# Performance work log

Hardware: AMD Instinct MI355X
Metric: run time of the kernel (lower is better)

The kernel has to match this reference:

```python
import jax, jax.numpy as jnp
import numpy as np

HEAD_NUM = 16
EMBED = 1024
B, T = 2, 2048


def setup_inputs() -> dict:
    key = jax.random.key(0)
    k1, k2, k3 = jax.random.split(key, 3)
    x = jax.random.normal(k1, (B, T, EMBED), dtype=jnp.float32)
    # torch Linear weights: [out_features, in_features]; scaled like default init
    w_qkv = jax.random.normal(k2, (3 * EMBED, EMBED), dtype=jnp.float32) / np.sqrt(EMBED)
    w_out = jax.random.normal(k3, (EMBED, EMBED), dtype=jnp.float32) / np.sqrt(EMBED)
    return {"x": x, "w_qkv": w_qkv, "w_out": w_out}


def reference(x, w_qkv, w_out):
    b, t, e = x.shape
    h = HEAD_NUM
    d = e // h
    dk = d ** 0.5  # NOTE: original MULTIPLIES scores by sqrt(head_dim)
    qkv = x @ w_qkv.T  # [b, t, 3e]
    # einops 'b t (d k h) -> k b h t d' with k=3: split order is (d, 3, h)
    qkv = qkv.reshape(b, t, d, 3, h)
    qkv = jnp.transpose(qkv, (3, 0, 4, 1, 2))  # [3, b, h, t, d]
    q, k, v = qkv[0], qkv[1], qkv[2]
    energy = jnp.einsum('bhid,bhjd->bhij', q, k) * dk  # [b, h, t, t]
    attn = jax.nn.softmax(energy, axis=-1)
    out = jnp.einsum('bhij,bhjd->bhid', attn, v)  # [b, h, t, d]
    out = jnp.transpose(out, (0, 2, 1, 3)).reshape(b, t, e)  # b t (h d)
    return out @ w_out.T
```

## Files before the change

### kernel.cpp

```cpp
#include <hip/hip_runtime.h>
#include <hip/hip_bf16.h>

typedef _Float16 f16x8 __attribute__((ext_vector_type(8)));
typedef unsigned short u16x8 __attribute__((ext_vector_type(8)));
typedef unsigned short u16x4 __attribute__((ext_vector_type(4)));
typedef float f32x4 __attribute__((ext_vector_type(4)));

static constexpr int Bn = 2;
static constexpr int Tn = 2048;
static constexpr int En = 1024;
static constexpr int Hn = 16;
static constexpr int Dn = 64;
#define LOG2E 1.44269504088896340736f

static constexpr int TS = 136;
static constexpr int PS = 40;

__device__ __forceinline__ unsigned short f2h(float x) {
  _Float16 h = (_Float16)x;
  return __builtin_bit_cast(unsigned short, h);
}
__device__ __forceinline__ float h2f(unsigned short u) {
  return (float)__builtin_bit_cast(_Float16, u);
}
__device__ __forceinline__ f16x8 ldh8(const unsigned short* p) {
  return __builtin_bit_cast(f16x8, *reinterpret_cast<const u16x8*>(p));
}
__device__ __forceinline__ unsigned int pk2(float a, float b) {
  return __builtin_bit_cast(unsigned int, __builtin_amdgcn_cvt_pkrtz(a, b));
}
__device__ __forceinline__ void gld16(const void* g, void* l) {
  __builtin_amdgcn_global_load_lds(
      (__attribute__((address_space(1))) void*)(const_cast<void*>(g)),
      (__attribute__((address_space(3))) void*)(l), 16, 0, 0);
}

__global__ __launch_bounds__(256) void split_f32_f16(
    const float* __restrict__ src, unsigned short* __restrict__ hi,
    unsigned short* __restrict__ lo)
{
  const int i = (blockIdx.x * 256 + threadIdx.x) * 4;
  const float4 v = *reinterpret_cast<const float4*>(src + i);
  ushort4 h, l;
  h.x = f2h(v.x); l.x = f2h(v.x - h2f(h.x));
  h.y = f2h(v.y); l.y = f2h(v.y - h2f(h.y));
  h.z = f2h(v.z); l.z = f2h(v.z - h2f(h.z));
  h.w = f2h(v.w); l.w = f2h(v.w - h2f(h.w));
  *reinterpret_cast<ushort4*>(hi + i) = h;
  *reinterpret_cast<ushort4*>(lo + i) = l;
}

__global__ __launch_bounds__(256) void cvt_f32_f16(
    const float* __restrict__ src, unsigned short* __restrict__ dst)
{
  const int i = (blockIdx.x * 256 + threadIdx.x) * 4;
  const float4 v = *reinterpret_cast<const float4*>(src + i);
  ushort4 u;
  u.x = f2h(v.x); u.y = f2h(v.y); u.z = f2h(v.z); u.w = f2h(v.w);
  *reinterpret_cast<ushort4*>(dst + i) = u;
}

__global__ __launch_bounds__(256) void gemm_qkv(
    const unsigned short* __restrict__ xh, const unsigned short* __restrict__ xl,
    const unsigned short* __restrict__ wf,
    unsigned short* __restrict__ Qf, unsigned short* __restrict__ Kf,
    unsigned short* __restrict__ Vf, int M, int K)
{
  __shared__ unsigned short smem[2 * 12288];

  const int tid = threadIdx.x;
  const int w = tid >> 6, L = tid & 63, qd = L >> 4, lr = L & 15;
  const int m0 = blockIdx.y * 128;
  const int kk = blockIdx.x >> 3;
  const int hh0 = (blockIdx.x & 7) * 2;
  const int wm = (w >> 1) * 64, wn = (w & 1) * 64;

  size_t aoffs[2], boffs[2];
  int lbase[2];
#pragma unroll
  for (int p = 0; p < 2; ++p) {
    const int c = p * 256 + tid;
    const int row = c >> 2, slot = c & 3;
    const int dd = row & 63, hl = row >> 6;
    aoffs[p] = (size_t)(m0 + row) * K + slot * 8;
    boffs[p] = (size_t)(dd * 48 + kk * 16 + hh0 + hl) * K + slot * 8;
    lbase[p] = (p * 4 + w) * 512;
  }

  f32x4 acc[4][4] = {};

#pragma unroll
  for (int p = 0; p < 2; ++p) {
    gld16(xh + aoffs[p], &smem[lbase[p]]);
    gld16(wf + boffs[p], &smem[8192 + lbase[p]]);
    if (kk < 2) gld16(xl + aoffs[p], &smem[4096 + lbase[p]]);
  }
  __syncthreads();

  int buf = 0;
  for (int k0 = 0; k0 < K; k0 += 32) {
    if (k0 + 32 < K) {
      const int nb = (buf ^ 1) * 12288;
#pragma unroll
      for (int p = 0; p < 2; ++p) {
        gld16(xh + aoffs[p] + k0 + 32, &smem[nb + lbase[p]]);
        gld16(wf + boffs[p] + k0 + 32, &smem[nb + 8192 + lbase[p]]);
        if (kk < 2) gld16(xl + aoffs[p] + k0 + 32, &smem[nb + 4096 + lbase[p]]);
      }
    }

    const int cb = buf * 12288;
    f16x8 afh[4], bf[4];
#pragma unroll
    for (int mt = 0; mt < 4; ++mt)
      afh[mt] = ldh8(&smem[cb + (wm + mt * 16 + lr) * 32 + qd * 8]);
#pragma unroll
    for (int nt = 0; nt < 4; ++nt)
      bf[nt] = ldh8(&smem[cb + 8192 + (wn + nt * 16 + lr) * 32 + qd * 8]);
    if (kk < 2) {
      f16x8 afl[4];
#pragma unroll
      for (int mt = 0; mt < 4; ++mt)
        afl[mt] = ldh8(&smem[cb + 4096 + (wm + mt * 16 + lr) * 32 + qd * 8]);
#pragma unroll
      for (int mt = 0; mt < 4; ++mt)
#pragma unroll
        for (int nt = 0; nt < 4; ++nt) {
          acc[mt][nt] = __builtin_amdgcn_mfma_f32_16x16x32_f16(afh[mt], bf[nt], acc[mt][nt], 0, 0, 0);
          acc[mt][nt] = __builtin_amdgcn_mfma_f32_16x16x32_f16(afl[mt], bf[nt], acc[mt][nt], 0, 0, 0);
        }
    } else {
#pragma unroll
      for (int mt = 0; mt < 4; ++mt)
#pragma unroll
        for (int nt = 0; nt < 4; ++nt)
          acc[mt][nt] = __builtin_amdgcn_mfma_f32_16x16x32_f16(afh[mt], bf[nt], acc[mt][nt], 0, 0, 0);
    }
    __syncthreads();
    buf ^= 1;
  }

  const int b = m0 >> 11;
  const int t0 = m0 & (Tn - 1);
  const float qscale = (kk == 0) ? 8.0f * LOG2E : 1.0f;
#pragma unroll
  for (int mt = 0; mt < 4; ++mt)
#pragma unroll
    for (int nt = 0; nt < 4; ++nt)
#pragma unroll
      for (int r = 0; r < 4; ++r) {
        const int ml = wm + mt * 16 + qd * 4 + r;
        const int cl = wn + nt * 16 + lr;
        smem[ml * TS + cl] = f2h(acc[mt][nt][r] * qscale);
      }
  __syncthreads();

  unsigned short* dst = (kk == 0) ? Qf : (kk == 1) ? Kf : Vf;
  if (kk < 2) {
#pragma unroll
    for (int p = 0; p < 8; ++p) {
      const int s = p * 256 + tid;
      const int tl = s >> 4, sub = s & 15;
      const int hl = sub >> 3, oct = sub & 7;
      const u16x8 v = *reinterpret_cast<const u16x8*>(&smem[tl * TS + hl * 64 + oct * 8]);
      *reinterpret_cast<u16x8*>(
          dst + ((size_t)(b * Hn + hh0 + hl) * Tn + t0 + tl) * Dn + oct * 8) = v;
    }
  } else {
#pragma unroll
    for (int p = 0; p < 8; ++p) {
      const int s = p * 256 + tid;
      const int cl = s >> 4, oct = s & 15;
      const int hl = cl >> 6, dd = cl & 63;
      u16x8 v;
#pragma unroll
      for (int j = 0; j < 8; ++j) v[j] = smem[(oct * 8 + j) * TS + cl];
      *reinterpret_cast<u16x8*>(
          dst + ((size_t)((b * Hn + hh0 + hl) * Dn + dd)) * Tn + t0 + oct * 8) = v;
    }
  }
}

__global__ __launch_bounds__(256, 2) void attn_kernel(
    const unsigned short* __restrict__ Qf, const unsigned short* __restrict__ Kf,
    const unsigned short* __restrict__ Vf, unsigned short* __restrict__ AOf)
{
  __shared__ unsigned short shK[2 * 128 * 32];
  __shared__ unsigned short shV[4 * 64 * 32];
  __shared__ unsigned short shP[4 * 16 * PS];
  const int tid = threadIdx.x;
  const int w = tid >> 6, L = tid & 63, qd = L >> 4, lr = L & 15;
  const int q0 = blockIdx.x * 64;
  const int bh = blockIdx.y;
  unsigned short* myP = &shP[w * 16 * PS];

  f16x8 aq[2];
  {
    const size_t qoff = ((size_t)bh * Tn + q0 + w * 16 + lr) * Dn;
    aq[0] = ldh8(Qf + qoff + qd * 8);
    aq[1] = ldh8(Qf + qoff + 32 + qd * 8);
  }
  f16x8 ones;
#pragma unroll
  for (int j = 0; j < 8; ++j) ones[j] = (_Float16)1.0f;

  f32x4 oacc[4] = {};
  float mrow = -1e30f, lsum = 0.f;

  for (int j0 = 0; j0 < Tn; j0 += 128) {
#pragma unroll
    for (int p = 0; p < 4; ++p) {
      const int kc = p >> 1, half = p & 1;
      const int row = half * 64 + (tid >> 2);
      const int slot = tid & 3;
      gld16(Kf + ((size_t)bh * Tn + j0 + row) * Dn + kc * 32 + slot * 8,
            &shK[kc * 4096 + (half * 64 + w * 16) * 32]);
    }
#pragma unroll
    for (int p = 0; p < 4; ++p) {
      const int dd = tid >> 2, slot = tid & 3;
      gld16(Vf + ((size_t)bh * Dn + dd) * Tn + j0 + p * 32 + slot * 8,
            &shV[p * 2048 + (w * 16) * 32]);
    }
    __syncthreads();

    f32x4 s2[8];
#pragma unroll
    for (int ct = 0; ct < 8; ++ct) {
      const int rk = ct * 16 + lr;
      s2[ct] = f32x4{0.f, 0.f, 0.f, 0.f};
#pragma unroll
      for (int kc = 0; kc < 2; ++kc) {
        const f16x8 bk = ldh8(&shK[kc * 4096 + rk * 32 + qd * 8]);
        s2[ct] = __builtin_amdgcn_mfma_f32_16x16x32_f16(bk, aq[kc], s2[ct], 0, 0, 0);
      }
    }

    float tm = s2[0][0];
#pragma unroll
    for (int ct = 0; ct < 8; ++ct)
#pragma unroll
      for (int r = 0; r < 4; ++r) tm = fmaxf(tm, s2[ct][r]);
    tm = fmaxf(tm, __shfl_xor(tm, 16, 64));
    tm = fmaxf(tm, __shfl_xor(tm, 32, 64));
    const float mn = fmaxf(mrow, tm);
    const float alpha = exp2f(mrow - mn);
    mrow = mn;
#pragma unroll
    for (int ct = 0; ct < 8; ++ct)
#pragma unroll
      for (int r = 0; r < 4; ++r)
        s2[ct][r] = exp2f(s2[ct][r] - mrow);
#pragma unroll
    for (int nt = 0; nt < 4; ++nt)
#pragma unroll
      for (int r = 0; r < 4; ++r) oacc[nt][r] *= alpha;

    f32x4 sacc = {};
#pragma unroll
    for (int kcv = 0; kcv < 4; ++kcv) {
#pragma unroll
      for (int c2 = 0; c2 < 2; ++c2) {
        const int ct = kcv * 2 + c2;
        uint2 d2;
        d2.x = pk2(s2[ct][0], s2[ct][1]);
        d2.y = pk2(s2[ct][2], s2[ct][3]);
        *reinterpret_cast<uint2*>(&myP[lr * PS + c2 * 16 + qd * 4]) = d2;
      }
      const f16x8 pa = ldh8(&myP[lr * PS + qd * 8]);
#pragma unroll
      for (int nt = 0; nt < 4; ++nt) {
        const f16x8 bv = ldh8(&shV[kcv * 2048 + (nt * 16 + lr) * 32 + qd * 8]);
        oacc[nt] = __builtin_amdgcn_mfma_f32_16x16x32_f16(bv, pa, oacc[nt], 0, 0, 0);
      }
      sacc = __builtin_amdgcn_mfma_f32_16x16x32_f16(ones, pa, sacc, 0, 0, 0);
    }
    lsum = lsum * alpha + sacc[0];
    __syncthreads();
  }

  const int b = bh >> 4, h = bh & 15;
  const float inv = 1.0f / lsum;
  const int q = q0 + w * 16 + lr;
#pragma unroll
  for (int nt = 0; nt < 4; ++nt) {
    unsigned short o[4];
#pragma unroll
    for (int r = 0; r < 4; ++r) o[r] = f2h(oacc[nt][r] * inv);
    const int col = h * 64 + nt * 16 + qd * 4;
    *reinterpret_cast<u16x4*>(&AOf[((size_t)b * Tn + q) * En + col]) =
        u16x4{o[0], o[1], o[2], o[3]};
  }
}

__global__ __launch_bounds__(256) void gemm_out(
    const unsigned short* __restrict__ A, const unsigned short* __restrict__ Bm,
    float* __restrict__ C, int M, int N, int K)
{
  __shared__ unsigned short shA[128 * 32];
  __shared__ unsigned short shB[128 * 32];
  const int tid = threadIdx.x;
  const int w = tid >> 6, L = tid & 63, qd = L >> 4, lr = L & 15;
  const int m0 = blockIdx.y * 128;
  const int n0 = blockIdx.x * 128;
  const int wm = (w >> 1) * 64, wn = (w & 1) * 64;

  f32x4 acc[4][4] = {};

  for (int k0 = 0; k0 < K; k0 += 32) {
#pragma unroll
    for (int p = 0; p < 2; ++p) {
      const int c = p * 256 + tid;
      const int row = c >> 2, slot = c & 3;
      const int base = (p * 4 + w) * 512;
      gld16(A + (size_t)(m0 + row) * K + k0 + slot * 8, &shA[base]);
      gld16(Bm + (size_t)(n0 + row) * K + k0 + slot * 8, &shB[base]);
    }
    __syncthreads();

    f16x8 af[4], bf[4];
#pragma unroll
    for (int mt = 0; mt < 4; ++mt)
      af[mt] = ldh8(&shA[(wm + mt * 16 + lr) * 32 + qd * 8]);
#pragma unroll
    for (int nt = 0; nt < 4; ++nt)
      bf[nt] = ldh8(&shB[(wn + nt * 16 + lr) * 32 + qd * 8]);
#pragma unroll
    for (int mt = 0; mt < 4; ++mt)
#pragma unroll
      for (int nt = 0; nt < 4; ++nt)
        acc[mt][nt] = __builtin_amdgcn_mfma_f32_16x16x32_f16(af[mt], bf[nt], acc[mt][nt], 0, 0, 0);
    __syncthreads();
  }

#pragma unroll
  for (int mt = 0; mt < 4; ++mt)
#pragma unroll
    for (int nt = 0; nt < 4; ++nt)
#pragma unroll
      for (int r = 0; r < 4; ++r) {
        const int m = m0 + wm + mt * 16 + qd * 4 + r;
        const int n = n0 + wn + nt * 16 + lr;
        C[(size_t)m * N + n] = acc[mt][nt][r];
      }
}

extern "C" void kernel_launch(void* const* d_in, const int* in_sizes, int n_in,
                              void* d_out, int out_size, void* d_ws, size_t ws_size,
                              hipStream_t stream) {
  (void)in_sizes; (void)n_in; (void)out_size; (void)ws_size;
  const float* x = (const float*)d_in[0];
  const float* wqkv = (const float*)d_in[1];
  const float* wout = (const float*)d_in[2];
  float* out = (float*)d_out;

  const size_t elems = (size_t)Bn * Hn * Tn * Dn;
  unsigned short* Qf = (unsigned short*)d_ws;
  unsigned short* Kf = Qf + elems;
  unsigned short* Vf = Kf + elems;
  unsigned short* AOf = Vf + elems;
  unsigned short* wf = AOf + elems;
  unsigned short* wof = wf + (size_t)3 * En * En;

  unsigned short* xh = (unsigned short*)d_out;
  unsigned short* xl = xh + elems;

  const int M = Bn * Tn;
  dim3 blk(256);
  split_f32_f16<<<dim3((int)(elems / 1024)), blk, 0, stream>>>(x, xh, xl);
  cvt_f32_f16<<<dim3(3 * En * En / 1024), blk, 0, stream>>>(wqkv, wf);
  cvt_f32_f16<<<dim3(En * En / 1024), blk, 0, stream>>>(wout, wof);
  gemm_qkv<<<dim3(24, M / 128), blk, 0, stream>>>(
      xh, xl, wf, Qf, Kf, Vf, M, En);
  attn_kernel<<<dim3(Tn / 64, Bn * Hn), blk, 0, stream>>>(Qf, Kf, Vf, AOf);
  gemm_out<<<dim3(En / 128, M / 128), blk, 0, stream>>>(
      AOf, wof, out, M, En, En);
}
```

Baseline: 245.7 us.

## Double-buffer K/V tiles in attention to overlap global loads with MFMA

```diff
diff --git a/kernel.cpp b/kernel.cpp
--- a/kernel.cpp
+++ b/kernel.cpp
@@ -185,8 +185,8 @@
     const unsigned short* __restrict__ Qf, const unsigned short* __restrict__ Kf,
     const unsigned short* __restrict__ Vf, unsigned short* __restrict__ AOf)
 {
-  __shared__ unsigned short shK[2 * 128 * 32];
-  __shared__ unsigned short shV[4 * 64 * 32];
+  __shared__ unsigned short shK[2 * 2 * 128 * 32];
+  __shared__ unsigned short shV[2 * 4 * 64 * 32];
   __shared__ unsigned short shP[4 * 16 * PS];
   const int tid = threadIdx.x;
   const int w = tid >> 6, L = tid & 63, qd = L >> 4, lr = L & 15;
@@ -204,25 +204,45 @@
 #pragma unroll
   for (int j = 0; j < 8; ++j) ones[j] = (_Float16)1.0f;
 
+  const int krow = tid >> 2, kslot = tid & 3;
+  const size_t Kb = (size_t)bh * Tn;
+  const size_t Vb = (size_t)bh * Dn;
+
   f32x4 oacc[4] = {};
   float mrow = -1e30f, lsum = 0.f;
 
+#pragma unroll
+  for (int p = 0; p < 4; ++p) {
+    const int kc = p >> 1, half = p & 1;
+    gld16(Kf + (Kb + half * 64 + krow) * Dn + kc * 32 + kslot * 8,
+          &shK[kc * 4096 + (half * 64 + w * 16) * 32]);
+  }
+#pragma unroll
+  for (int p = 0; p < 4; ++p) {
+    gld16(Vf + (Vb + krow) * Tn + p * 32 + kslot * 8,
+          &shV[p * 2048 + (w * 16) * 32]);
+  }
+  __syncthreads();
+
+  int buf = 0;
   for (int j0 = 0; j0 < Tn; j0 += 128) {
-#pragma unroll
-    for (int p = 0; p < 4; ++p) {
-      const int kc = p >> 1, half = p & 1;
-      const int row = half * 64 + (tid >> 2);
-      const int slot = tid & 3;
-      gld16(Kf + ((size_t)bh * Tn + j0 + row) * Dn + kc * 32 + slot * 8,
-            &shK[kc * 4096 + (half * 64 + w * 16) * 32]);
-    }
-#pragma unroll
-    for (int p = 0; p < 4; ++p) {
-      const int dd = tid >> 2, slot = tid & 3;
-      gld16(Vf + ((size_t)bh * Dn + dd) * Tn + j0 + p * 32 + slot * 8,
-            &shV[p * 2048 + (w * 16) * 32]);
-    }
-    __syncthreads();
+    if (j0 + 128 < Tn) {
+      const int nbK = (buf ^ 1) * 8192;
+      const int nbV = (buf ^ 1) * 8192;
+#pragma unroll
+      for (int p = 0; p < 4; ++p) {
+        const int kc = p >> 1, half = p & 1;
+        gld16(Kf + (Kb + j0 + 128 + half * 64 + krow) * Dn + kc * 32 + kslot * 8,
+              &shK[nbK + kc * 4096 + (half * 64 + w * 16) * 32]);
+      }
+#pragma unroll
+      for (int p = 0; p < 4; ++p) {
+        gld16(Vf + (Vb + krow) * Tn + j0 + 128 + p * 32 + kslot * 8,
+              &shV[nbV + p * 2048 + (w * 16) * 32]);
+      }
+    }
+
+    const int cbK = buf * 8192, cbV = buf * 8192;
 
     f32x4 s2[8];
 #pragma unroll
@@ -231,7 +251,7 @@
       s2[ct] = f32x4{0.f, 0.f, 0.f, 0.f};
 #pragma unroll
       for (int kc = 0; kc < 2; ++kc) {
-        const f16x8 bk = ldh8(&shK[kc * 4096 + rk * 32 + qd * 8]);
+        const f16x8 bk = ldh8(&shK[cbK + kc * 4096 + rk * 32 + qd * 8]);
         s2[ct] = __builtin_amdgcn_mfma_f32_16x16x32_f16(bk, aq[kc], s2[ct], 0, 0, 0);
       }
     }
@@ -270,13 +290,14 @@
       const f16x8 pa = ldh8(&myP[lr * PS + qd * 8]);
 #pragma unroll
       for (int nt = 0; nt < 4; ++nt) {
-        const f16x8 bv = ldh8(&shV[kcv * 2048 + (nt * 16 + lr) * 32 + qd * 8]);
+        const f16x8 bv = ldh8(&shV[cbV + kcv * 2048 + (nt * 16 + lr) * 32 + qd * 8]);
         oacc[nt] = __builtin_amdgcn_mfma_f32_16x16x32_f16(bv, pa, oacc[nt], 0, 0, 0);
       }
       sacc = __builtin_amdgcn_mfma_f32_16x16x32_f16(ones, pa, sacc, 0, 0, 0);
     }
     lsum = lsum * alpha + sacc[0];
     __syncthreads();
+    buf ^= 1;
   }
 
   const int b = bh >> 4, h = bh & 15;
```

Result: slower. 253.5 us (+3.2%).
